# Kernel optimization log

Measured on AMD Instinct MI355X. Metric: run time of the kernel, lower is better.

The kernel has to match this reference:

```python
import jax, jax.numpy as jnp
import numpy as np

G, IN_D, OUT_D, KQ_D = 8192, 512, 512, 128
EPS = 1e-12  # torch F.normalize default eps


def setup_inputs() -> dict:
    key = jax.random.key(0)
    ks = jax.random.split(key, 7)
    s_in = 1.0 / np.sqrt(IN_D)
    return {
        "x": jax.random.normal(ks[0], (G, IN_D), dtype=jnp.float32),
        "Wk": jax.random.uniform(ks[1], (KQ_D, IN_D), jnp.float32, -s_in, s_in),
        "bk": jax.random.uniform(ks[2], (KQ_D,), jnp.float32, -s_in, s_in),
        "Wq": jax.random.uniform(ks[3], (KQ_D, IN_D), jnp.float32, -s_in, s_in),
        "bq": jax.random.uniform(ks[4], (KQ_D,), jnp.float32, -s_in, s_in),
        "Wv": jax.random.uniform(ks[5], (OUT_D, IN_D), jnp.float32, -s_in, s_in),
        "bv": jax.random.uniform(ks[6], (OUT_D,), jnp.float32, -s_in, s_in),
    }


def reference(x, Wk, bk, Wq, bq, Wv, bv):
    # QKV projections (torch Linear: x @ W^T + b)
    k = x @ Wk.T + bk            # [g, kq]
    q = x @ Wq.T + bq            # [g, kq]
    v = x @ Wv.T + bv            # [g, outD]
    # g x g attention scores
    scores = k @ q.T             # [g, g]
    # L2-normalize each row (F.normalize with dim=-1): x / max(||x||_2, eps)
    norm = jnp.sqrt(jnp.sum(scores * scores, axis=-1, keepdims=True))
    scores_n = scores / jnp.maximum(norm, EPS)
    # value matmul + residual
    return scores_n @ v + v      # [g, outD]
```

## Files before the change

### kernel.cpp

```cpp
#include <hip/hip_runtime.h>
#include <hip/hip_bf16.h>
#include <stdint.h>

typedef __attribute__((ext_vector_type(8))) short bf16x8;
typedef __attribute__((ext_vector_type(4))) float f32x4;

__device__ __forceinline__ unsigned short f2bf(float f) {
  union { float f; uint32_t u; } v; v.f = f;
  uint32_t u = v.u;
  return (unsigned short)((u + 0x7fffu + ((u >> 16) & 1u)) >> 16);
}
__device__ __forceinline__ float bf2f(unsigned short h) {
  union { uint32_t u; float f; } v; v.u = ((uint32_t)h) << 16;
  return v.f;
}

#define GLL(g, l) __builtin_amdgcn_global_load_lds( \
    (const __attribute__((address_space(1))) void*)(g), \
    (__attribute__((address_space(3))) void*)(l), 16, 0, 0)

__global__ void cvt_all(const float* __restrict__ x,
                        const float* __restrict__ wk, const float* __restrict__ wq,
                        const float* __restrict__ wv,
                        unsigned short* __restrict__ xb, unsigned short* __restrict__ wb) {
  const int i = (blockIdx.x * 256 + threadIdx.x) * 4;
  const float* src; unsigned short* dst; int off;
  if (i < 4194304) { src = x; dst = xb; off = i; }
  else {
    const int j = i - 4194304;
    if (j < 65536)       { src = wk; off = j; }
    else if (j < 131072) { src = wq; off = j - 65536; }
    else                 { src = wv; off = j - 131072; }
    dst = wb + (j - off);
  }
  const float4 v = *(const float4*)(src + off);
  ushort4 o; o.x = f2bf(v.x); o.y = f2bf(v.y); o.z = f2bf(v.z); o.w = f2bf(v.w);
  *(ushort4*)(dst + off) = o;
}

__global__ __launch_bounds__(256, 3) void qkv_gemm(
    const unsigned short* __restrict__ xb, const unsigned short* __restrict__ wb,
    const float* __restrict__ pbk, const float* __restrict__ pbq, const float* __restrict__ pbv,
    unsigned short* __restrict__ kb, unsigned short* __restrict__ qtb,
    unsigned short* __restrict__ vb, unsigned short* __restrict__ vtb)
{
  __shared__ unsigned short Alds[2][64 * 64];
  __shared__ unsigned short Blds[2][128 * 64];
  const int tid = threadIdx.x;
  const int lane = tid & 63;
  const int wid = tid >> 6;
  const int wm = wid >> 1, wn = wid & 1;
  const int wg = blockIdx.x;
  const int s = (wg & 7) * 96 + (wg >> 3);
  const int bx = s & 127, by = s >> 7;
  const int m0 = bx * 64, n0 = by * 128;
  const int l15 = lane & 15, l4 = lane >> 4;

  f32x4 acc[2][4] = {};

  auto stage = [&](int b, int kt) {
    const int k0 = kt * 64;
    #pragma unroll
    for (int p = 0; p < 2; ++p) {
      const int e = p * 256 + tid;
      const int row = e >> 3;
      const int cs = (e & 7) ^ (row & 7);
      GLL(xb + (size_t)(m0 + row) * 512 + k0 + cs * 8, &Alds[b][(p * 256 + (tid & ~63)) * 8]);
    }
    #pragma unroll
    for (int p = 0; p < 4; ++p) {
      const int e = p * 256 + tid;
      const int row = e >> 3;
      const int cs = (e & 7) ^ (row & 7);
      GLL(wb + (size_t)(n0 + row) * 512 + k0 + cs * 8, &Blds[b][(p * 256 + (tid & ~63)) * 8]);
    }
  };

  stage(0, 0);
  __syncthreads();

  for (int kt = 0; kt < 8; ++kt) {
    const int cur = kt & 1;
    if (kt < 7) stage(cur ^ 1, kt + 1);
    #pragma unroll
    for (int kk = 0; kk < 2; ++kk) {
      bf16x8 af[2], bfv[4];
      #pragma unroll
      for (int i = 0; i < 2; ++i) {
        const int ra = wm * 32 + i * 16 + l15;
        const int c  = kk * 4 + l4;
        af[i] = *(const bf16x8*)(&Alds[cur][ra * 64 + ((c ^ (ra & 7)) * 8)]);
      }
      #pragma unroll
      for (int j = 0; j < 4; ++j) {
        const int rb = wn * 64 + j * 16 + l15;
        const int c  = kk * 4 + l4;
        bfv[j] = *(const bf16x8*)(&Blds[cur][rb * 64 + ((c ^ (rb & 7)) * 8)]);
      }
      #pragma unroll
      for (int i = 0; i < 2; ++i)
        #pragma unroll
        for (int j = 0; j < 4; ++j)
          acc[i][j] = __builtin_amdgcn_mfma_f32_16x16x32_bf16(af[i], bfv[j], acc[i][j], 0, 0, 0);
    }
    __syncthreads();
  }

  #pragma unroll
  for (int i = 0; i < 2; ++i) {
    #pragma unroll
    for (int j = 0; j < 4; ++j) {
      const int rbase = m0 + wm * 32 + i * 16 + l4 * 4;
      const int c = n0 + wn * 64 + j * 16 + l15;
      const float bias = (c < 128) ? pbk[c] : (c < 256) ? pbq[c - 128] : pbv[c - 256];
      unsigned short o[4];
      #pragma unroll
      for (int r = 0; r < 4; ++r) o[r] = f2bf(acc[i][j][r] + bias);
      if (c < 128) {
        #pragma unroll
        for (int r = 0; r < 4; ++r) kb[(size_t)(rbase + r) * 128 + c] = o[r];
      } else if (c < 256) {
        ushort4 t; t.x = o[0]; t.y = o[1]; t.z = o[2]; t.w = o[3];
        *(ushort4*)(qtb + (size_t)(c - 128) * 8192 + rbase) = t;
      } else {
        #pragma unroll
        for (int r = 0; r < 4; ++r) vb[(size_t)(rbase + r) * 512 + (c - 256)] = o[r];
        ushort4 t; t.x = o[0]; t.y = o[1]; t.z = o[2]; t.w = o[3];
        *(ushort4*)(vtb + (size_t)(c - 256) * 8192 + rbase) = t;
      }
    }
  }
}

__global__ __launch_bounds__(512) void gh_gemm(
    const unsigned short* __restrict__ qtb, const unsigned short* __restrict__ vtb,
    unsigned short* __restrict__ pb)
{
  __shared__ unsigned short Alds[2][128 * 64];
  __shared__ unsigned short Blds[2][80 * 64];
  const int tid = threadIdx.x, lane = tid & 63, wid = tid >> 6;
  const int l15 = lane & 15, l4 = lane >> 4;
  const int kc = blockIdx.x, nq = blockIdx.y;
  const int g0 = kc * 256;
  const int m0 = wid * 16;

  f32x4 acc[5] = {};

  auto stage = [&](int b, int st) {
    const int gs = g0 + st * 64;
    #pragma unroll
    for (int p = 0; p < 2; ++p) {
      const int e = p * 512 + tid;
      const int row = e >> 3;
      const int cs = (e & 7) ^ (row & 7);
      GLL(qtb + (size_t)row * 8192 + gs + cs * 8, &Alds[b][(p * 512 + (tid & ~63)) * 8]);
    }
    {
      const int row = tid >> 3;
      const int cglob = nq * 80 + row;
      const unsigned short* src = (cglob < 128) ? (qtb + (size_t)cglob * 8192)
                                                : (vtb + (size_t)(cglob - 128) * 8192);
      const int cs = (tid & 7) ^ (row & 7);
      GLL(src + gs + cs * 8, &Blds[b][(tid & ~63) * 8]);
    }
    if (tid < 128) {
      const int e = 512 + tid;
      const int row = e >> 3;
      const int cglob = nq * 80 + row;
      const unsigned short* src = (cglob < 128) ? (qtb + (size_t)cglob * 8192)
                                                : (vtb + (size_t)(cglob - 128) * 8192);
      const int cs = (e & 7) ^ (row & 7);
      GLL(src + gs + cs * 8, &Blds[b][(512 + (tid & ~63)) * 8]);
    }
  };

  stage(0, 0);
  __syncthreads();

  for (int st = 0; st < 4; ++st) {
    const int cur = st & 1;
    if (st < 3) stage(cur ^ 1, st + 1);
    #pragma unroll
    for (int ks = 0; ks < 2; ++ks) {
      const int ra = m0 + l15;
      const int ca = ks * 4 + l4;
      const bf16x8 af = *(const bf16x8*)(&Alds[cur][ra * 64 + ((ca ^ (ra & 7)) * 8)]);
      #pragma unroll
      for (int nf = 0; nf < 5; ++nf) {
        const int rb = nf * 16 + l15;
        const bf16x8 bf = *(const bf16x8*)(&Blds[cur][rb * 64 + ((ca ^ (rb & 7)) * 8)]);
        acc[nf] = __builtin_amdgcn_mfma_f32_16x16x32_bf16(af, bf, acc[nf], 0, 0, 0);
      }
    }
    __syncthreads();
  }

  #pragma unroll
  for (int nf = 0; nf < 5; ++nf) {
    const int col = nq * 80 + nf * 16 + l15;
    #pragma unroll
    for (int r = 0; r < 4; ++r) {
      const int row = m0 + l4 * 4 + r;
      pb[((size_t)kc * 128 + row) * 640 + col] = f2bf(acc[nf][r]);
    }
  }
}

__global__ void gh_finalize(const unsigned short* __restrict__ pb,
                            unsigned short* __restrict__ Gb, unsigned short* __restrict__ Hbt) {
  const int idx = blockIdx.x * 256 + threadIdx.x;
  float s = 0.f;
  #pragma unroll
  for (int p = 0; p < 32; ++p) s += bf2f(pb[(size_t)p * 81920 + idx]);
  const int m = idx / 640, c = idx % 640;
  if (c < 128) Gb[m * 128 + c] = f2bf(s);
  else         Hbt[(size_t)(c - 128) * 128 + m] = f2bf(s);
}

__global__ __launch_bounds__(512) void tnorm_uv(
    const unsigned short* __restrict__ kb, const unsigned short* __restrict__ Gb,
    const unsigned short* __restrict__ Hbt, const unsigned short* __restrict__ vb,
    float* __restrict__ out)
{
  __shared__ float ssq_part[8][16];
  __shared__ float rnorm_lds[16];
  const int tid = threadIdx.x, lane = tid & 63, wid = tid >> 6;
  const int l15 = lane & 15, l4 = lane >> 4;
  const int rowbase = blockIdx.x * 16;

  bf16x8 af[4];
  #pragma unroll
  for (int ks = 0; ks < 4; ++ks)
    af[ks] = *(const bf16x8*)(kb + (size_t)(rowbase + l15) * 128 + ks * 32 + l4 * 8);

  f32x4 tac = {};
  #pragma unroll
  for (int ks = 0; ks < 4; ++ks) {
    const bf16x8 bf = *(const bf16x8*)(Gb + (size_t)(wid * 16 + l15) * 128 + ks * 32 + l4 * 8);
    tac = __builtin_amdgcn_mfma_f32_16x16x32_bf16(af[ks], bf, tac, 0, 0, 0);
  }
  float ssq[4];
  #pragma unroll
  for (int r = 0; r < 4; ++r) {
    const int row = rowbase + l4 * 4 + r;
    ssq[r] = tac[r] * bf2f(kb[(size_t)row * 128 + wid * 16 + l15]);
  }
  #pragma unroll
  for (int d = 1; d < 16; d <<= 1)
    #pragma unroll
    for (int r = 0; r < 4; ++r) ssq[r] += __shfl_xor(ssq[r], d);
  if (l15 == 0) {
    #pragma unroll
    for (int r = 0; r < 4; ++r) ssq_part[wid][l4 * 4 + r] = ssq[r];
  }
  __syncthreads();
  if (tid < 16) {
    float s = 0.f;
    #pragma unroll
    for (int w = 0; w < 8; ++w) s += ssq_part[w][tid];
    rnorm_lds[tid] = 1.0f / fmaxf(sqrtf(s), 1e-12f);
  }
  __syncthreads();

  f32x4 acc[4] = {};
  #pragma unroll
  for (int ks = 0; ks < 4; ++ks) {
    #pragma unroll
    for (int nf = 0; nf < 4; ++nf) {
      const int col = wid * 64 + nf * 16 + l15;
      const bf16x8 bf = *(const bf16x8*)(Hbt + (size_t)col * 128 + ks * 32 + l4 * 8);
      acc[nf] = __builtin_amdgcn_mfma_f32_16x16x32_bf16(af[ks], bf, acc[nf], 0, 0, 0);
    }
  }

  float rn[4];
  #pragma unroll
  for (int r = 0; r < 4; ++r) rn[r] = rnorm_lds[l4 * 4 + r];

  #pragma unroll
  for (int nf = 0; nf < 4; ++nf) {
    const int col = wid * 64 + nf * 16 + l15;
    #pragma unroll
    for (int r = 0; r < 4; ++r) {
      const int row = rowbase + l4 * 4 + r;
      out[(size_t)row * 512 + col] =
          acc[nf][r] * rn[r] + bf2f(vb[(size_t)row * 512 + col]);
    }
  }
}

extern "C" void kernel_launch(void* const* d_in, const int* in_sizes, int n_in,
                              void* d_out, int out_size, void* d_ws, size_t ws_size,
                              hipStream_t stream) {
  const float* x  = (const float*)d_in[0];
  const float* Wk = (const float*)d_in[1];
  const float* bk = (const float*)d_in[2];
  const float* Wq = (const float*)d_in[3];
  const float* bq = (const float*)d_in[4];
  const float* Wv = (const float*)d_in[5];
  const float* bv = (const float*)d_in[6];
  float* out = (float*)d_out;

  char* ws = (char*)d_ws;
  unsigned short* xb   = (unsigned short*)(ws);
  unsigned short* wb   = (unsigned short*)(ws + 8388608);
  unsigned short* kb   = (unsigned short*)(ws + 9175040);
  unsigned short* vb   = (unsigned short*)(ws + 11272192);
  unsigned short* vtb  = (unsigned short*)(ws + 19660800);
  unsigned short* qtb  = (unsigned short*)(ws + 28049408);
  unsigned short* pb   = (unsigned short*)(ws + 30146560);
  unsigned short* Gb   = (unsigned short*)(ws + 35389440);
  unsigned short* Hbt  = (unsigned short*)(ws + 35422208);

  cvt_all<<<4480, 256, 0, stream>>>(x, Wk, Wq, Wv, xb, wb);
  qkv_gemm<<<768, 256, 0, stream>>>(xb, wb, bk, bq, bv, kb, qtb, vb, vtb);
  gh_gemm<<<dim3(32, 8), 512, 0, stream>>>(qtb, vtb, pb);
  gh_finalize<<<320, 256, 0, stream>>>(pb, Gb, Hbt);
  tnorm_uv<<<512, 512, 0, stream>>>(kb, Gb, Hbt, vb, out);
}
```

Measured before the change: 52.37 us.

## Fuse fp32-to-bf16 conversion into QKV GEMM staging and drop convert kernel

Removes the separate cvt_all kernel. The QKV GEMM now loads fp32 x and weights into registers, converts them to bf16 and writes them into swizzled LDS after the MFMA work, so the next tile's global loads overlap compute. This drops a full launch and the bf16 round trip of x through memory, at the cost of more registers and global_load_lds being replaced by manual LDS stores. In the final kernel it also hoists the residual v loads ahead of the norm-reduction barrier.

```diff
diff --git a/kernel.cpp b/kernel.cpp
--- a/kernel.cpp
+++ b/kernel.cpp
@@ -19,27 +19,9 @@
     (const __attribute__((address_space(1))) void*)(g), \
     (__attribute__((address_space(3))) void*)(l), 16, 0, 0)
 
-__global__ void cvt_all(const float* __restrict__ x,
-                        const float* __restrict__ wk, const float* __restrict__ wq,
-                        const float* __restrict__ wv,
-                        unsigned short* __restrict__ xb, unsigned short* __restrict__ wb) {
-  const int i = (blockIdx.x * 256 + threadIdx.x) * 4;
-  const float* src; unsigned short* dst; int off;
-  if (i < 4194304) { src = x; dst = xb; off = i; }
-  else {
-    const int j = i - 4194304;
-    if (j < 65536)       { src = wk; off = j; }
-    else if (j < 131072) { src = wq; off = j - 65536; }
-    else                 { src = wv; off = j - 131072; }
-    dst = wb + (j - off);
-  }
-  const float4 v = *(const float4*)(src + off);
-  ushort4 o; o.x = f2bf(v.x); o.y = f2bf(v.y); o.z = f2bf(v.z); o.w = f2bf(v.w);
-  *(ushort4*)(dst + off) = o;
-}
-
 __global__ __launch_bounds__(256, 3) void qkv_gemm(
-    const unsigned short* __restrict__ xb, const unsigned short* __restrict__ wb,
+    const float* __restrict__ x,
+    const float* __restrict__ wk, const float* __restrict__ wq, const float* __restrict__ wv,
     const float* __restrict__ pbk, const float* __restrict__ pbq, const float* __restrict__ pbv,
     unsigned short* __restrict__ kb, unsigned short* __restrict__ qtb,
     unsigned short* __restrict__ vb, unsigned short* __restrict__ vtb)
@@ -53,49 +35,72 @@
   const int wg = blockIdx.x;
   const int s = (wg & 7) * 96 + (wg >> 3);
   const int bx = s & 127, by = s >> 7;
-  const int m0 = bx * 64, n0 = by * 128;
+  const int m0 = bx * 64;
   const int l15 = lane & 15, l4 = lane >> 4;
 
+  const float* wsrc; const float* bsrc; int nrow0;
+  if (by == 0)      { wsrc = wk; bsrc = pbk; nrow0 = 0; }
+  else if (by == 1) { wsrc = wq; bsrc = pbq; nrow0 = 0; }
+  else              { wsrc = wv; bsrc = pbv; nrow0 = (by - 2) * 128; }
+
   f32x4 acc[2][4] = {};
-
-  auto stage = [&](int b, int kt) {
+  float4 ra[4], rb[8];
+
+  auto loadregs = [&](int kt) {
     const int k0 = kt * 64;
     #pragma unroll
-    for (int p = 0; p < 2; ++p) {
-      const int e = p * 256 + tid;
-      const int row = e >> 3;
-      const int cs = (e & 7) ^ (row & 7);
-      GLL(xb + (size_t)(m0 + row) * 512 + k0 + cs * 8, &Alds[b][(p * 256 + (tid & ~63)) * 8]);
-    }
-    #pragma unroll
     for (int p = 0; p < 4; ++p) {
-      const int e = p * 256 + tid;
-      const int row = e >> 3;
-      const int cs = (e & 7) ^ (row & 7);
-      GLL(wb + (size_t)(n0 + row) * 512 + k0 + cs * 8, &Blds[b][(p * 256 + (tid & ~63)) * 8]);
+      const int h = p * 256 + tid;
+      const int row = h >> 4, hw = h & 15;
+      ra[p] = *(const float4*)(x + (size_t)(m0 + row) * 512 + k0 + hw * 4);
+    }
+    #pragma unroll
+    for (int p = 0; p < 8; ++p) {
+      const int h = p * 256 + tid;
+      const int row = h >> 4, hw = h & 15;
+      rb[p] = *(const float4*)(wsrc + (size_t)(nrow0 + row) * 512 + k0 + hw * 4);
     }
   };
-
-  stage(0, 0);
+  auto cvtwrite = [&](int b) {
+    #pragma unroll
+    for (int p = 0; p < 4; ++p) {
+      const int h = p * 256 + tid;
+      const int row = h >> 4, hw = h & 15;
+      const int ci = hw >> 1, part = hw & 1;
+      ushort4 o; o.x = f2bf(ra[p].x); o.y = f2bf(ra[p].y); o.z = f2bf(ra[p].z); o.w = f2bf(ra[p].w);
+      *(ushort4*)((char*)&Alds[b][0] + row * 128 + ((ci ^ (row & 7)) * 16) + part * 8) = o;
+    }
+    #pragma unroll
+    for (int p = 0; p < 8; ++p) {
+      const int h = p * 256 + tid;
+      const int row = h >> 4, hw = h & 15;
+      const int ci = hw >> 1, part = hw & 1;
+      ushort4 o; o.x = f2bf(rb[p].x); o.y = f2bf(rb[p].y); o.z = f2bf(rb[p].z); o.w = f2bf(rb[p].w);
+      *(ushort4*)((char*)&Blds[b][0] + row * 128 + ((ci ^ (row & 7)) * 16) + part * 8) = o;
+    }
+  };
+
+  loadregs(0);
+  cvtwrite(0);
   __syncthreads();
 
   for (int kt = 0; kt < 8; ++kt) {
     const int cur = kt & 1;
-    if (kt < 7) stage(cur ^ 1, kt + 1);
+    if (kt < 7) loadregs(kt + 1);
     #pragma unroll
     for (int kk = 0; kk < 2; ++kk) {
       bf16x8 af[2], bfv[4];
       #pragma unroll
       for (int i = 0; i < 2; ++i) {
-        const int ra = wm * 32 + i * 16 + l15;
+        const int ra_ = wm * 32 + i * 16 + l15;
         const int c  = kk * 4 + l4;
-        af[i] = *(const bf16x8*)(&Alds[cur][ra * 64 + ((c ^ (ra & 7)) * 8)]);
+        af[i] = *(const bf16x8*)(&Alds[cur][ra_ * 64 + ((c ^ (ra_ & 7)) * 8)]);
       }
       #pragma unroll
       for (int j = 0; j < 4; ++j) {
-        const int rb = wn * 64 + j * 16 + l15;
+        const int rb_ = wn * 64 + j * 16 + l15;
         const int c  = kk * 4 + l4;
-        bfv[j] = *(const bf16x8*)(&Blds[cur][rb * 64 + ((c ^ (rb & 7)) * 8)]);
+        bfv[j] = *(const bf16x8*)(&Blds[cur][rb_ * 64 + ((c ^ (rb_ & 7)) * 8)]);
       }
       #pragma unroll
       for (int i = 0; i < 2; ++i)
@@ -103,6 +108,7 @@
         for (int j = 0; j < 4; ++j)
           acc[i][j] = __builtin_amdgcn_mfma_f32_16x16x32_bf16(af[i], bfv[j], acc[i][j], 0, 0, 0);
     }
+    if (kt < 7) cvtwrite(cur ^ 1);
     __syncthreads();
   }
 
@@ -111,22 +117,23 @@
     #pragma unroll
     for (int j = 0; j < 4; ++j) {
       const int rbase = m0 + wm * 32 + i * 16 + l4 * 4;
-      const int c = n0 + wn * 64 + j * 16 + l15;
-      const float bias = (c < 128) ? pbk[c] : (c < 256) ? pbq[c - 128] : pbv[c - 256];
+      const int c = wn * 64 + j * 16 + l15;
+      const float bias = bsrc[nrow0 + c];
       unsigned short o[4];
       #pragma unroll
       for (int r = 0; r < 4; ++r) o[r] = f2bf(acc[i][j][r] + bias);
-      if (c < 128) {
+      if (by == 0) {
         #pragma unroll
         for (int r = 0; r < 4; ++r) kb[(size_t)(rbase + r) * 128 + c] = o[r];
-      } else if (c < 256) {
+      } else if (by == 1) {
         ushort4 t; t.x = o[0]; t.y = o[1]; t.z = o[2]; t.w = o[3];
-        *(ushort4*)(qtb + (size_t)(c - 128) * 8192 + rbase) = t;
+        *(ushort4*)(qtb + (size_t)c * 8192 + rbase) = t;
       } else {
+        const int vcol = nrow0 + c;
         #pragma unroll
-        for (int r = 0; r < 4; ++r) vb[(size_t)(rbase + r) * 512 + (c - 256)] = o[r];
+        for (int r = 0; r < 4; ++r) vb[(size_t)(rbase + r) * 512 + vcol] = o[r];
         ushort4 t; t.x = o[0]; t.y = o[1]; t.z = o[2]; t.w = o[3];
-        *(ushort4*)(vtb + (size_t)(c - 256) * 8192 + rbase) = t;
+        *(ushort4*)(vtb + (size_t)vcol * 8192 + rbase) = t;
       }
     }
   }
@@ -253,14 +260,6 @@
     #pragma unroll
     for (int r = 0; r < 4; ++r) ssq_part[wid][l4 * 4 + r] = ssq[r];
   }
-  __syncthreads();
-  if (tid < 16) {
-    float s = 0.f;
-    #pragma unroll
-    for (int w = 0; w < 8; ++w) s += ssq_part[w][tid];
-    rnorm_lds[tid] = 1.0f / fmaxf(sqrtf(s), 1e-12f);
-  }
-  __syncthreads();
 
   f32x4 acc[4] = {};
   #pragma unroll
@@ -272,19 +271,35 @@
       acc[nf] = __builtin_amdgcn_mfma_f32_16x16x32_bf16(af[ks], bf, acc[nf], 0, 0, 0);
     }
   }
-
-  float rn[4];
-  #pragma unroll
-  for (int r = 0; r < 4; ++r) rn[r] = rnorm_lds[l4 * 4 + r];
-
+  float vres[4][4];
   #pragma unroll
   for (int nf = 0; nf < 4; ++nf) {
     const int col = wid * 64 + nf * 16 + l15;
     #pragma unroll
+    for (int r = 0; r < 4; ++r)
+      vres[nf][r] = bf2f(vb[(size_t)(rowbase + l4 * 4 + r) * 512 + col]);
+  }
+
+  __syncthreads();
+  if (tid < 16) {
+    float s = 0.f;
+    #pragma unroll
+    for (int w = 0; w < 8; ++w) s += ssq_part[w][tid];
+    rnorm_lds[tid] = 1.0f / fmaxf(sqrtf(s), 1e-12f);
+  }
+  __syncthreads();
+
+  float rn[4];
+  #pragma unroll
+  for (int r = 0; r < 4; ++r) rn[r] = rnorm_lds[l4 * 4 + r];
+
+  #pragma unroll
+  for (int nf = 0; nf < 4; ++nf) {
+    const int col = wid * 64 + nf * 16 + l15;
+    #pragma unroll
     for (int r = 0; r < 4; ++r) {
       const int row = rowbase + l4 * 4 + r;
-      out[(size_t)row * 512 + col] =
-          acc[nf][r] * rn[r] + bf2f(vb[(size_t)row * 512 + col]);
+      out[(size_t)row * 512 + col] = acc[nf][r] * rn[r] + vres[nf][r];
     }
   }
 }
@@ -302,18 +317,15 @@
   float* out = (float*)d_out;
 
   char* ws = (char*)d_ws;
-  unsigned short* xb   = (unsigned short*)(ws);
-  unsigned short* wb   = (unsigned short*)(ws + 8388608);
-  unsigned short* kb   = (unsigned short*)(ws + 9175040);
-  unsigned short* vb   = (unsigned short*)(ws + 11272192);
-  unsigned short* vtb  = (unsigned short*)(ws + 19660800);
-  unsigned short* qtb  = (unsigned short*)(ws + 28049408);
-  unsigned short* pb   = (unsigned short*)(ws + 30146560);
-  unsigned short* Gb   = (unsigned short*)(ws + 35389440);
-  unsigned short* Hbt  = (unsigned short*)(ws + 35422208);
-
-  cvt_all<<<4480, 256, 0, stream>>>(x, Wk, Wq, Wv, xb, wb);
-  qkv_gemm<<<768, 256, 0, stream>>>(xb, wb, bk, bq, bv, kb, qtb, vb, vtb);
+  unsigned short* kb   = (unsigned short*)(ws);
+  unsigned short* vb   = (unsigned short*)(ws + 2097152);
+  unsigned short* vtb  = (unsigned short*)(ws + 10485760);
+  unsigned short* qtb  = (unsigned short*)(ws + 18874368);
+  unsigned short* pb   = (unsigned short*)(ws + 20971520);
+  unsigned short* Gb   = (unsigned short*)(ws + 26214400);
+  unsigned short* Hbt  = (unsigned short*)(ws + 26247168);
+
+  qkv_gemm<<<768, 256, 0, stream>>>(x, Wk, Wq, Wv, bk, bq, bv, kb, qtb, vb, vtb);
   gh_gemm<<<dim3(32, 8), 512, 0, stream>>>(qtb, vtb, pb);
   gh_finalize<<<320, 256, 0, stream>>>(pb, Gb, Hbt);
   tnorm_uv<<<512, 512, 0, stream>>>(kb, Gb, Hbt, vb, out);
```

After: 68.55 us. 1.31x slower.

## Fuse G/H gemm, reduction and normalize-output into one cooperative kernel

Applied to the files above, without the earlier changes.

Merges the three trailing kernels (partial Q^T[Q|V] gemm, split-K reduction, and row-norm plus output gemm) into a single cooperative kernel of 256 blocks that uses grid-wide syncs between phases. The final phase is re-tiled to 32 rows per block with 8 waves, each covering 128 output columns, and it prefetches the residual V before the block barrier. This removes two kernel launches and their inter-kernel gaps, at the cost of grid.sync overhead and fewer blocks in the last phase.

```diff
diff --git a/kernel.cpp b/kernel.cpp
--- a/kernel.cpp
+++ b/kernel.cpp
@@ -1,6 +1,9 @@
 #include <hip/hip_runtime.h>
 #include <hip/hip_bf16.h>
+#include <hip/hip_cooperative_groups.h>
 #include <stdint.h>
+
+namespace cg = cooperative_groups;
 
 typedef __attribute__((ext_vector_type(8))) short bf16x8;
 typedef __attribute__((ext_vector_type(4))) float f32x4;
@@ -123,168 +126,192 @@
         ushort4 t; t.x = o[0]; t.y = o[1]; t.z = o[2]; t.w = o[3];
         *(ushort4*)(qtb + (size_t)(c - 128) * 8192 + rbase) = t;
       } else {
+        const int vcol = c - 256;
         #pragma unroll
-        for (int r = 0; r < 4; ++r) vb[(size_t)(rbase + r) * 512 + (c - 256)] = o[r];
+        for (int r = 0; r < 4; ++r) vb[(size_t)(rbase + r) * 512 + vcol] = o[r];
         ushort4 t; t.x = o[0]; t.y = o[1]; t.z = o[2]; t.w = o[3];
-        *(ushort4*)(vtb + (size_t)(c - 256) * 8192 + rbase) = t;
-      }
-    }
-  }
-}
-
-__global__ __launch_bounds__(512) void gh_gemm(
+        *(ushort4*)(vtb + (size_t)vcol * 8192 + rbase) = t;
+      }
+    }
+  }
+}
+
+__global__ __launch_bounds__(512) void gh_all(
     const unsigned short* __restrict__ qtb, const unsigned short* __restrict__ vtb,
-    unsigned short* __restrict__ pb)
+    const unsigned short* __restrict__ kb, const unsigned short* __restrict__ vb,
+    unsigned short* __restrict__ pb, unsigned short* __restrict__ Gb,
+    unsigned short* __restrict__ Hbt, float* __restrict__ out)
 {
   __shared__ unsigned short Alds[2][128 * 64];
   __shared__ unsigned short Blds[2][80 * 64];
+  __shared__ float ssq_part[4][32];
+  __shared__ float rnorm_lds[32];
+
+  cg::grid_group grid = cg::this_grid();
   const int tid = threadIdx.x, lane = tid & 63, wid = tid >> 6;
   const int l15 = lane & 15, l4 = lane >> 4;
-  const int kc = blockIdx.x, nq = blockIdx.y;
-  const int g0 = kc * 256;
-  const int m0 = wid * 16;
-
-  f32x4 acc[5] = {};
-
-  auto stage = [&](int b, int st) {
-    const int gs = g0 + st * 64;
-    #pragma unroll
-    for (int p = 0; p < 2; ++p) {
-      const int e = p * 512 + tid;
-      const int row = e >> 3;
-      const int cs = (e & 7) ^ (row & 7);
-      GLL(qtb + (size_t)row * 8192 + gs + cs * 8, &Alds[b][(p * 512 + (tid & ~63)) * 8]);
-    }
-    {
-      const int row = tid >> 3;
-      const int cglob = nq * 80 + row;
-      const unsigned short* src = (cglob < 128) ? (qtb + (size_t)cglob * 8192)
-                                                : (vtb + (size_t)(cglob - 128) * 8192);
-      const int cs = (tid & 7) ^ (row & 7);
-      GLL(src + gs + cs * 8, &Blds[b][(tid & ~63) * 8]);
-    }
-    if (tid < 128) {
-      const int e = 512 + tid;
-      const int row = e >> 3;
-      const int cglob = nq * 80 + row;
-      const unsigned short* src = (cglob < 128) ? (qtb + (size_t)cglob * 8192)
-                                                : (vtb + (size_t)(cglob - 128) * 8192);
-      const int cs = (e & 7) ^ (row & 7);
-      GLL(src + gs + cs * 8, &Blds[b][(512 + (tid & ~63)) * 8]);
-    }
-  };
-
-  stage(0, 0);
-  __syncthreads();
-
-  for (int st = 0; st < 4; ++st) {
-    const int cur = st & 1;
-    if (st < 3) stage(cur ^ 1, st + 1);
-    #pragma unroll
-    for (int ks = 0; ks < 2; ++ks) {
-      const int ra = m0 + l15;
-      const int ca = ks * 4 + l4;
-      const bf16x8 af = *(const bf16x8*)(&Alds[cur][ra * 64 + ((ca ^ (ra & 7)) * 8)]);
-      #pragma unroll
-      for (int nf = 0; nf < 5; ++nf) {
-        const int rb = nf * 16 + l15;
-        const bf16x8 bf = *(const bf16x8*)(&Blds[cur][rb * 64 + ((ca ^ (rb & 7)) * 8)]);
-        acc[nf] = __builtin_amdgcn_mfma_f32_16x16x32_bf16(af, bf, acc[nf], 0, 0, 0);
-      }
-    }
+  const int bid = blockIdx.x;
+
+  {
+    const int kc = bid & 31, nq = bid >> 5;
+    const int g0 = kc * 256;
+    const int m0 = wid * 16;
+
+    f32x4 acc[5] = {};
+
+    auto stage = [&](int b, int st) {
+      const int gs = g0 + st * 64;
+      #pragma unroll
+      for (int p = 0; p < 2; ++p) {
+        const int e = p * 512 + tid;
+        const int row = e >> 3;
+        const int cs = (e & 7) ^ (row & 7);
+        GLL(qtb + (size_t)row * 8192 + gs + cs * 8, &Alds[b][(p * 512 + (tid & ~63)) * 8]);
+      }
+      {
+        const int row = tid >> 3;
+        const int cglob = nq * 80 + row;
+        const unsigned short* src = (cglob < 128) ? (qtb + (size_t)cglob * 8192)
+                                                  : (vtb + (size_t)(cglob - 128) * 8192);
+        const int cs = (tid & 7) ^ (row & 7);
+        GLL(src + gs + cs * 8, &Blds[b][(tid & ~63) * 8]);
+      }
+      if (tid < 128) {
+        const int e = 512 + tid;
+        const int row = e >> 3;
+        const int cglob = nq * 80 + row;
+        const unsigned short* src = (cglob < 128) ? (qtb + (size_t)cglob * 8192)
+                                                  : (vtb + (size_t)(cglob - 128) * 8192);
+        const int cs = (e & 7) ^ (row & 7);
+        GLL(src + gs + cs * 8, &Blds[b][(512 + (tid & ~63)) * 8]);
+      }
+    };
+
+    stage(0, 0);
     __syncthreads();
-  }
-
-  #pragma unroll
-  for (int nf = 0; nf < 5; ++nf) {
-    const int col = nq * 80 + nf * 16 + l15;
-    #pragma unroll
-    for (int r = 0; r < 4; ++r) {
-      const int row = m0 + l4 * 4 + r;
-      pb[((size_t)kc * 128 + row) * 640 + col] = f2bf(acc[nf][r]);
-    }
-  }
-}
-
-__global__ void gh_finalize(const unsigned short* __restrict__ pb,
-                            unsigned short* __restrict__ Gb, unsigned short* __restrict__ Hbt) {
-  const int idx = blockIdx.x * 256 + threadIdx.x;
-  float s = 0.f;
-  #pragma unroll
-  for (int p = 0; p < 32; ++p) s += bf2f(pb[(size_t)p * 81920 + idx]);
-  const int m = idx / 640, c = idx % 640;
-  if (c < 128) Gb[m * 128 + c] = f2bf(s);
-  else         Hbt[(size_t)(c - 128) * 128 + m] = f2bf(s);
-}
-
-__global__ __launch_bounds__(512) void tnorm_uv(
-    const unsigned short* __restrict__ kb, const unsigned short* __restrict__ Gb,
-    const unsigned short* __restrict__ Hbt, const unsigned short* __restrict__ vb,
-    float* __restrict__ out)
-{
-  __shared__ float ssq_part[8][16];
-  __shared__ float rnorm_lds[16];
-  const int tid = threadIdx.x, lane = tid & 63, wid = tid >> 6;
-  const int l15 = lane & 15, l4 = lane >> 4;
-  const int rowbase = blockIdx.x * 16;
-
-  bf16x8 af[4];
-  #pragma unroll
-  for (int ks = 0; ks < 4; ++ks)
-    af[ks] = *(const bf16x8*)(kb + (size_t)(rowbase + l15) * 128 + ks * 32 + l4 * 8);
-
-  f32x4 tac = {};
-  #pragma unroll
-  for (int ks = 0; ks < 4; ++ks) {
-    const bf16x8 bf = *(const bf16x8*)(Gb + (size_t)(wid * 16 + l15) * 128 + ks * 32 + l4 * 8);
-    tac = __builtin_amdgcn_mfma_f32_16x16x32_bf16(af[ks], bf, tac, 0, 0, 0);
-  }
-  float ssq[4];
-  #pragma unroll
-  for (int r = 0; r < 4; ++r) {
-    const int row = rowbase + l4 * 4 + r;
-    ssq[r] = tac[r] * bf2f(kb[(size_t)row * 128 + wid * 16 + l15]);
-  }
-  #pragma unroll
-  for (int d = 1; d < 16; d <<= 1)
-    #pragma unroll
-    for (int r = 0; r < 4; ++r) ssq[r] += __shfl_xor(ssq[r], d);
-  if (l15 == 0) {
-    #pragma unroll
-    for (int r = 0; r < 4; ++r) ssq_part[wid][l4 * 4 + r] = ssq[r];
-  }
-  __syncthreads();
-  if (tid < 16) {
-    float s = 0.f;
-    #pragma unroll
-    for (int w = 0; w < 8; ++w) s += ssq_part[w][tid];
-    rnorm_lds[tid] = 1.0f / fmaxf(sqrtf(s), 1e-12f);
-  }
-  __syncthreads();
-
-  f32x4 acc[4] = {};
-  #pragma unroll
-  for (int ks = 0; ks < 4; ++ks) {
-    #pragma unroll
-    for (int nf = 0; nf < 4; ++nf) {
-      const int col = wid * 64 + nf * 16 + l15;
-      const bf16x8 bf = *(const bf16x8*)(Hbt + (size_t)col * 128 + ks * 32 + l4 * 8);
-      acc[nf] = __builtin_amdgcn_mfma_f32_16x16x32_bf16(af[ks], bf, acc[nf], 0, 0, 0);
-    }
-  }
-
-  float rn[4];
-  #pragma unroll
-  for (int r = 0; r < 4; ++r) rn[r] = rnorm_lds[l4 * 4 + r];
-
-  #pragma unroll
-  for (int nf = 0; nf < 4; ++nf) {
-    const int col = wid * 64 + nf * 16 + l15;
-    #pragma unroll
-    for (int r = 0; r < 4; ++r) {
-      const int row = rowbase + l4 * 4 + r;
-      out[(size_t)row * 512 + col] =
-          acc[nf][r] * rn[r] + bf2f(vb[(size_t)row * 512 + col]);
+
+    for (int st = 0; st < 4; ++st) {
+      const int cur = st & 1;
+      if (st < 3) stage(cur ^ 1, st + 1);
+      #pragma unroll
+      for (int ks = 0; ks < 2; ++ks) {
+        const int ra = m0 + l15;
+        const int ca = ks * 4 + l4;
+        const bf16x8 af = *(const bf16x8*)(&Alds[cur][ra * 64 + ((ca ^ (ra & 7)) * 8)]);
+        #pragma unroll
+        for (int nf = 0; nf < 5; ++nf) {
+          const int rb = nf * 16 + l15;
+          const bf16x8 bf = *(const bf16x8*)(&Blds[cur][rb * 64 + ((ca ^ (rb & 7)) * 8)]);
+          acc[nf] = __builtin_amdgcn_mfma_f32_16x16x32_bf16(af, bf, acc[nf], 0, 0, 0);
+        }
+      }
+      __syncthreads();
+    }
+
+    #pragma unroll
+    for (int nf = 0; nf < 5; ++nf) {
+      const int col = nq * 80 + nf * 16 + l15;
+      #pragma unroll
+      for (int r = 0; r < 4; ++r) {
+        const int row = m0 + l4 * 4 + r;
+        pb[((size_t)kc * 128 + row) * 640 + col] = f2bf(acc[nf][r]);
+      }
+    }
+  }
+
+  grid.sync();
+
+  {
+    const int idx = bid * 512 + tid;
+    if (idx < 81920) {
+      float s = 0.f;
+      #pragma unroll
+      for (int p = 0; p < 32; ++p) s += bf2f(pb[(size_t)p * 81920 + idx]);
+      const int m = idx / 640, c = idx % 640;
+      if (c < 128) Gb[m * 128 + c] = f2bf(s);
+      else         Hbt[(size_t)(c - 128) * 128 + m] = f2bf(s);
+    }
+  }
+
+  grid.sync();
+
+  {
+    const int m0 = bid * 32;
+    const int mf = wid & 1, nq = wid >> 1;
+    const int rowbase = m0 + mf * 16;
+
+    bf16x8 af[4];
+    #pragma unroll
+    for (int ks = 0; ks < 4; ++ks)
+      af[ks] = *(const bf16x8*)(kb + (size_t)(rowbase + l15) * 128 + ks * 32 + l4 * 8);
+
+    f32x4 tac[2] = {};
+    #pragma unroll
+    for (int ks = 0; ks < 4; ++ks) {
+      #pragma unroll
+      for (int t = 0; t < 2; ++t) {
+        const int nf = nq * 2 + t;
+        const bf16x8 bf = *(const bf16x8*)(Gb + (size_t)(nf * 16 + l15) * 128 + ks * 32 + l4 * 8);
+        tac[t] = __builtin_amdgcn_mfma_f32_16x16x32_bf16(af[ks], bf, tac[t], 0, 0, 0);
+      }
+    }
+    float ssq[4] = {0.f, 0.f, 0.f, 0.f};
+    #pragma unroll
+    for (int t = 0; t < 2; ++t) {
+      const int col = (nq * 2 + t) * 16 + l15;
+      #pragma unroll
+      for (int r = 0; r < 4; ++r) {
+        const int row = rowbase + l4 * 4 + r;
+        ssq[r] += tac[t][r] * bf2f(kb[(size_t)row * 128 + col]);
+      }
+    }
+    #pragma unroll
+    for (int d = 1; d < 16; d <<= 1)
+      #pragma unroll
+      for (int r = 0; r < 4; ++r) ssq[r] += __shfl_xor(ssq[r], d);
+    if (l15 == 0) {
+      #pragma unroll
+      for (int r = 0; r < 4; ++r) ssq_part[nq][mf * 16 + l4 * 4 + r] = ssq[r];
+    }
+
+    f32x4 acc[8] = {};
+    #pragma unroll
+    for (int ks = 0; ks < 4; ++ks) {
+      #pragma unroll
+      for (int nf = 0; nf < 8; ++nf) {
+        const int col = nq * 128 + nf * 16 + l15;
+        const bf16x8 bf = *(const bf16x8*)(Hbt + (size_t)col * 128 + ks * 32 + l4 * 8);
+        acc[nf] = __builtin_amdgcn_mfma_f32_16x16x32_bf16(af[ks], bf, acc[nf], 0, 0, 0);
+      }
+    }
+    float vres[8][4];
+    #pragma unroll
+    for (int nf = 0; nf < 8; ++nf) {
+      const int col = nq * 128 + nf * 16 + l15;
+      #pragma unroll
+      for (int r = 0; r < 4; ++r)
+        vres[nf][r] = bf2f(vb[(size_t)(rowbase + l4 * 4 + r) * 512 + col]);
+    }
+
+    __syncthreads();
+    if (tid < 32) {
+      const float s = ssq_part[0][tid] + ssq_part[1][tid] + ssq_part[2][tid] + ssq_part[3][tid];
+      rnorm_lds[tid] = 1.0f / fmaxf(sqrtf(s), 1e-12f);
+    }
+    __syncthreads();
+
+    float rn[4];
+    #pragma unroll
+    for (int r = 0; r < 4; ++r) rn[r] = rnorm_lds[mf * 16 + l4 * 4 + r];
+
+    #pragma unroll
+    for (int nf = 0; nf < 8; ++nf) {
+      const int col = nq * 128 + nf * 16 + l15;
+      #pragma unroll
+      for (int r = 0; r < 4; ++r) {
+        const int row = rowbase + l4 * 4 + r;
+        out[(size_t)row * 512 + col] = acc[nf][r] * rn[r] + vres[nf][r];
+      }
     }
   }
 }
@@ -314,7 +341,10 @@
 
   cvt_all<<<4480, 256, 0, stream>>>(x, Wk, Wq, Wv, xb, wb);
   qkv_gemm<<<768, 256, 0, stream>>>(xb, wb, bk, bq, bv, kb, qtb, vb, vtb);
-  gh_gemm<<<dim3(32, 8), 512, 0, stream>>>(qtb, vtb, pb);
-  gh_finalize<<<320, 256, 0, stream>>>(pb, Gb, Hbt);
-  tnorm_uv<<<512, 512, 0, stream>>>(kb, Gb, Hbt, vb, out);
-}
+
+  const unsigned short* qtb_c = qtb; const unsigned short* vtb_c = vtb;
+  const unsigned short* kb_c = kb;   const unsigned short* vb_c = vb;
+  void* args[] = { (void*)&qtb_c, (void*)&vtb_c, (void*)&kb_c, (void*)&vb_c,
+                   (void*)&pb, (void*)&Gb, (void*)&Hbt, (void*)&out };
+  hipLaunchCooperativeKernel((void*)gh_all, dim3(256), dim3(512), args, 0, stream);
+}
```

Measured after the change: 128.1 us. +144.7%, slower.

## Split fused norm/output kernel into LDS-tiled norm and output GEMM kernels

Applied to the files above, without the earlier changes.

The single tnorm_uv kernel, which read K, G and H^T straight from global memory for every 16-row block, is replaced by two kernels. A tnorm kernel computes per-row inverse norms over 128-row tiles, and a 2D-tiled uv_out kernel computes the K·H^T product with scaling and the residual add. Both stage their operand tiles in XOR-swizzled LDS using global_load_lds, so G and H^T are reused from shared memory instead of reloaded per block. The cost is an extra kernel launch, a round-trip of the norms through global memory, and only 64 blocks for the norm pass.

```diff
diff --git a/kernel.cpp b/kernel.cpp
--- a/kernel.cpp
+++ b/kernel.cpp
@@ -18,6 +18,7 @@
 #define GLL(g, l) __builtin_amdgcn_global_load_lds( \
     (const __attribute__((address_space(1))) void*)(g), \
     (__attribute__((address_space(3))) void*)(l), 16, 0, 0)
+#define WAITV0() asm volatile("s_waitcnt vmcnt(0)" ::: "memory")
 
 __global__ void cvt_all(const float* __restrict__ x,
                         const float* __restrict__ wk, const float* __restrict__ wq,
@@ -123,10 +124,11 @@
         ushort4 t; t.x = o[0]; t.y = o[1]; t.z = o[2]; t.w = o[3];
         *(ushort4*)(qtb + (size_t)(c - 128) * 8192 + rbase) = t;
       } else {
+        const int vcol = c - 256;
         #pragma unroll
-        for (int r = 0; r < 4; ++r) vb[(size_t)(rbase + r) * 512 + (c - 256)] = o[r];
+        for (int r = 0; r < 4; ++r) vb[(size_t)(rbase + r) * 512 + vcol] = o[r];
         ushort4 t; t.x = o[0]; t.y = o[1]; t.z = o[2]; t.w = o[3];
-        *(ushort4*)(vtb + (size_t)(c - 256) * 8192 + rbase) = t;
+        *(ushort4*)(vtb + (size_t)vcol * 8192 + rbase) = t;
       }
     }
   }
@@ -217,74 +219,127 @@
   else         Hbt[(size_t)(c - 128) * 128 + m] = f2bf(s);
 }
 
-__global__ __launch_bounds__(512) void tnorm_uv(
+__global__ __launch_bounds__(512, 2) void tnorm(
     const unsigned short* __restrict__ kb, const unsigned short* __restrict__ Gb,
-    const unsigned short* __restrict__ Hbt, const unsigned short* __restrict__ vb,
+    float* __restrict__ rnm)
+{
+  __shared__ unsigned short Kld[128 * 128];
+  __shared__ unsigned short Gld[128 * 128];
+  const int tid = threadIdx.x, lane = tid & 63, wid = tid >> 6;
+  const int l15 = lane & 15, l4 = lane >> 4;
+  const int m0 = blockIdx.x * 128;
+
+  #pragma unroll
+  for (int p = 0; p < 4; ++p) {
+    const int e = p * 512 + tid;
+    const int row = e >> 4, ch = e & 15;
+    const int cs = ch ^ ((row & 7) << 1);
+    GLL(kb + (size_t)(m0 + row) * 128 + cs * 8, &Kld[(e & ~63) * 8]);
+    GLL(Gb + (size_t)row * 128 + cs * 8,        &Gld[(e & ~63) * 8]);
+  }
+  WAITV0();
+  __syncthreads();
+
+  bf16x8 af[4];
+  #pragma unroll
+  for (int ks = 0; ks < 4; ++ks) {
+    const int row = wid * 16 + l15, ci = ks * 4 + l4;
+    af[ks] = *(const bf16x8*)((const char*)Kld + row * 256 + ((ci ^ ((row & 7) << 1)) * 16));
+  }
+  f32x4 tac[8] = {};
+  #pragma unroll
+  for (int ks = 0; ks < 4; ++ks) {
+    #pragma unroll
+    for (int nf = 0; nf < 8; ++nf) {
+      const int grow = nf * 16 + l15, ci = ks * 4 + l4;
+      const bf16x8 bf = *(const bf16x8*)((const char*)Gld + grow * 256 +
+                                         ((ci ^ ((grow & 7) << 1)) * 16));
+      tac[nf] = __builtin_amdgcn_mfma_f32_16x16x32_bf16(af[ks], bf, tac[nf], 0, 0, 0);
+    }
+  }
+
+  float ssq[4] = {0.f, 0.f, 0.f, 0.f};
+  #pragma unroll
+  for (int nf = 0; nf < 8; ++nf) {
+    #pragma unroll
+    for (int r = 0; r < 4; ++r) {
+      const int row = wid * 16 + l4 * 4 + r;
+      const int col = nf * 16 + l15;
+      const unsigned short kv = *(const unsigned short*)((const char*)Kld + row * 256 +
+          ((((col >> 3)) ^ ((row & 7) << 1)) * 16) + (col & 7) * 2);
+      ssq[r] += tac[nf][r] * bf2f(kv);
+    }
+  }
+  #pragma unroll
+  for (int d = 1; d < 16; d <<= 1)
+    #pragma unroll
+    for (int r = 0; r < 4; ++r) ssq[r] += __shfl_xor(ssq[r], d);
+  if (l15 == 0) {
+    #pragma unroll
+    for (int r = 0; r < 4; ++r)
+      rnm[m0 + wid * 16 + l4 * 4 + r] = 1.0f / fmaxf(sqrtf(ssq[r]), 1e-12f);
+  }
+}
+
+__global__ __launch_bounds__(512, 4) void uv_out(
+    const unsigned short* __restrict__ kb, const unsigned short* __restrict__ Hbt,
+    const float* __restrict__ rnm, const unsigned short* __restrict__ vb,
     float* __restrict__ out)
 {
-  __shared__ float ssq_part[8][16];
-  __shared__ float rnorm_lds[16];
+  __shared__ unsigned short Kld[128 * 128];
+  __shared__ unsigned short Hld[128 * 128];
   const int tid = threadIdx.x, lane = tid & 63, wid = tid >> 6;
   const int l15 = lane & 15, l4 = lane >> 4;
-  const int rowbase = blockIdx.x * 16;
-
-  bf16x8 af[4];
-  #pragma unroll
-  for (int ks = 0; ks < 4; ++ks)
-    af[ks] = *(const bf16x8*)(kb + (size_t)(rowbase + l15) * 128 + ks * 32 + l4 * 8);
-
-  f32x4 tac = {};
+  const int m0 = blockIdx.x * 128, n0 = blockIdx.y * 128;
+  const int wm = wid >> 2, wn = wid & 3;
+
+  #pragma unroll
+  for (int p = 0; p < 4; ++p) {
+    const int e = p * 512 + tid;
+    const int row = e >> 4, ch = e & 15;
+    const int cs = ch ^ ((row & 7) << 1);
+    GLL(kb  + (size_t)(m0 + row) * 128 + cs * 8, &Kld[(e & ~63) * 8]);
+    GLL(Hbt + (size_t)(n0 + row) * 128 + cs * 8, &Hld[(e & ~63) * 8]);
+  }
+  WAITV0();
+  __syncthreads();
+
+  f32x4 acc[4][2] = {};
   #pragma unroll
   for (int ks = 0; ks < 4; ++ks) {
-    const bf16x8 bf = *(const bf16x8*)(Gb + (size_t)(wid * 16 + l15) * 128 + ks * 32 + l4 * 8);
-    tac = __builtin_amdgcn_mfma_f32_16x16x32_bf16(af[ks], bf, tac, 0, 0, 0);
-  }
-  float ssq[4];
-  #pragma unroll
-  for (int r = 0; r < 4; ++r) {
-    const int row = rowbase + l4 * 4 + r;
-    ssq[r] = tac[r] * bf2f(kb[(size_t)row * 128 + wid * 16 + l15]);
-  }
-  #pragma unroll
-  for (int d = 1; d < 16; d <<= 1)
-    #pragma unroll
-    for (int r = 0; r < 4; ++r) ssq[r] += __shfl_xor(ssq[r], d);
-  if (l15 == 0) {
-    #pragma unroll
-    for (int r = 0; r < 4; ++r) ssq_part[wid][l4 * 4 + r] = ssq[r];
-  }
-  __syncthreads();
-  if (tid < 16) {
-    float s = 0.f;
-    #pragma unroll
-    for (int w = 0; w < 8; ++w) s += ssq_part[w][tid];
-    rnorm_lds[tid] = 1.0f / fmaxf(sqrtf(s), 1e-12f);
-  }
-  __syncthreads();
-
-  f32x4 acc[4] = {};
-  #pragma unroll
-  for (int ks = 0; ks < 4; ++ks) {
-    #pragma unroll
-    for (int nf = 0; nf < 4; ++nf) {
-      const int col = wid * 64 + nf * 16 + l15;
-      const bf16x8 bf = *(const bf16x8*)(Hbt + (size_t)col * 128 + ks * 32 + l4 * 8);
-      acc[nf] = __builtin_amdgcn_mfma_f32_16x16x32_bf16(af[ks], bf, acc[nf], 0, 0, 0);
-    }
-  }
-
-  float rn[4];
-  #pragma unroll
-  for (int r = 0; r < 4; ++r) rn[r] = rnorm_lds[l4 * 4 + r];
-
-  #pragma unroll
-  for (int nf = 0; nf < 4; ++nf) {
-    const int col = wid * 64 + nf * 16 + l15;
-    #pragma unroll
-    for (int r = 0; r < 4; ++r) {
-      const int row = rowbase + l4 * 4 + r;
-      out[(size_t)row * 512 + col] =
-          acc[nf][r] * rn[r] + bf2f(vb[(size_t)row * 512 + col]);
+    const int ci = ks * 4 + l4;
+    bf16x8 af[4], bf[2];
+    #pragma unroll
+    for (int i = 0; i < 4; ++i) {
+      const int row = wm * 64 + i * 16 + l15;
+      af[i] = *(const bf16x8*)((const char*)Kld + row * 256 + ((ci ^ ((row & 7) << 1)) * 16));
+    }
+    #pragma unroll
+    for (int j = 0; j < 2; ++j) {
+      const int col = wn * 32 + j * 16 + l15;
+      bf[j] = *(const bf16x8*)((const char*)Hld + col * 256 + ((ci ^ ((col & 7) << 1)) * 16));
+    }
+    #pragma unroll
+    for (int i = 0; i < 4; ++i)
+      #pragma unroll
+      for (int j = 0; j < 2; ++j)
+        acc[i][j] = __builtin_amdgcn_mfma_f32_16x16x32_bf16(af[i], bf[j], acc[i][j], 0, 0, 0);
+  }
+
+  #pragma unroll
+  for (int i = 0; i < 4; ++i) {
+    float rn[4];
+    #pragma unroll
+    for (int r = 0; r < 4; ++r) rn[r] = rnm[m0 + wm * 64 + i * 16 + l4 * 4 + r];
+    #pragma unroll
+    for (int j = 0; j < 2; ++j) {
+      const int col = n0 + wn * 32 + j * 16 + l15;
+      #pragma unroll
+      for (int r = 0; r < 4; ++r) {
+        const int row = m0 + wm * 64 + i * 16 + l4 * 4 + r;
+        out[(size_t)row * 512 + col] =
+            acc[i][j][r] * rn[r] + bf2f(vb[(size_t)row * 512 + col]);
+      }
     }
   }
 }
@@ -311,10 +366,12 @@
   unsigned short* pb   = (unsigned short*)(ws + 30146560);
   unsigned short* Gb   = (unsigned short*)(ws + 35389440);
   unsigned short* Hbt  = (unsigned short*)(ws + 35422208);
+  float*          rnm  = (float*)(ws + 35553280);
 
   cvt_all<<<4480, 256, 0, stream>>>(x, Wk, Wq, Wv, xb, wb);
   qkv_gemm<<<768, 256, 0, stream>>>(xb, wb, bk, bq, bv, kb, qtb, vb, vtb);
   gh_gemm<<<dim3(32, 8), 512, 0, stream>>>(qtb, vtb, pb);
   gh_finalize<<<320, 256, 0, stream>>>(pb, Gb, Hbt);
-  tnorm_uv<<<512, 512, 0, stream>>>(kb, Gb, Hbt, vb, out);
-}
+  tnorm<<<64, 512, 0, stream>>>(kb, Gb, rnm);
+  uv_out<<<dim3(64, 4), 512, 0, stream>>>(kb, Hbt, rnm, vb, out);
+}
```

Measured after the change: 48.86 us. -6.7%, faster.
